# Optimization experiments

Measured on AMD Instinct MI355X. Metric: run time of the kernel, lower is better.

## Reference

```python
import jax, jax.numpy as jnp
import numpy as np

EPS = 1e-05


def _nearest_upsample(x, H, W):
    # torch F.interpolate default mode='nearest': src_idx = floor(dst_idx * in/out)
    h, w = x.shape[-2], x.shape[-1]
    rows = (jnp.arange(H) * h) // H
    cols = (jnp.arange(W) * w) // W
    return x[..., rows[:, None], cols[None, :]]


def _dilate(mask, k):
    # Grayscale dilation with a flat (all-ones) k x k structuring element ==
    # k x k max filter (kornia dilation w/ ones kernel). Geodesic border: pad -inf
    p = (k - 1) // 2
    return jax.lax.reduce_window(
        mask, -jnp.inf, jax.lax.max,
        window_dimensions=(1, 1, k, k),
        window_strides=(1, 1, 1, 1),
        padding=[(0, 0), (0, 0), (p, k - 1 - p), (p, k - 1 - p)],
    )


def setup_inputs() -> dict:
    key = jax.random.key(0)
    k1, k2 = jax.random.split(key)
    small = jax.random.normal(k1, (2, 4, 1, 270, 480), dtype=jnp.float32)
    large = jax.random.uniform(k2, (2, 4, 1, 1080, 1920), dtype=jnp.float32)
    return {"small": small, "large": large, "dilate_width": 7, "sigmoid": 1}


def reference(small, large, dilate_width, sigmoid):
    B, T = small.shape[0], small.shape[1]
    s = small.reshape((B * T,) + small.shape[2:])   # [BT, C, h, w]
    l = large.reshape((B * T,) + large.shape[2:])   # [BT, C, H, W]
    H, W = l.shape[-2], l.shape[-1]
    up = _nearest_upsample(s, H, W)
    t = jax.nn.sigmoid(up) if sigmoid else up
    trans = ((t > EPS) & (t < 1.0 - EPS)).astype(l.dtype)
    if dilate_width >= 1:
        trans = _dilate(trans, dilate_width)
    out = trans * l + (1.0 - trans) * up
    return out.reshape(large.shape)
```

## Files before the change

### kernel.cpp

```cpp
#include <hip/hip_runtime.h>
#include <cmath>

#define HS 270
#define WS 480
#define HL 1080
#define WL 1920
#define W4 (WL / 4)

typedef float f4 __attribute__((ext_vector_type(4)));

__global__ __launch_bounds__(256) void PRM_77824807403842_kernel(
    const float* __restrict__ sml,
    const float* __restrict__ lrg,
    const int* __restrict__ sigp,
    float* __restrict__ out)
{
    const int n2 = blockIdx.x * 256 + threadIdx.x;
    const int bt = blockIdx.z;
    const int i = n2 / W4;
    const int p = n2 - i * W4;
    const int q = i >> 2;
    const int s = i & 3;

    const size_t lofs = ((size_t)bt * HL + i) * WL + 4 * (size_t)p;
    const f4 lv = *reinterpret_cast<const f4*>(lrg + lofs);

    const float* sb = sml + (size_t)bt * (HS * WS);
    const int rm = q > 0 ? q - 1 : 0;
    const int rp = q < HS - 1 ? q + 1 : q;
    const int cm = p > 0 ? p - 1 : 0;
    const int cp = p < WS - 1 ? p + 1 : p;
    const unsigned inc_t = (unsigned)((s < 3) & (q > 0));
    const unsigned inc_b = (unsigned)((s > 0) & (q < HS - 1));
    const unsigned vl = p > 0, vr = p < WS - 1;

    const float* r0 = sb + (size_t)rm * WS;
    const float* r1 = sb + (size_t)q * WS;
    const float* r2 = sb + (size_t)rp * WS;
    const float a0 = r0[cm], a1 = r0[p], a2 = r0[cp];
    const float b0 = r1[cm], b1 = r1[p], b2 = r1[cp];
    const float c0 = r2[cm], c1 = r2[p], c2 = r2[cp];

    const int sig = *sigp;
    auto msk = [&](float x) -> unsigned {
        return sig ? (unsigned)((x > -11.5129154f) & (x < 11.5129054f))
                   : (unsigned)((x > 1e-5f) & (x < 0.99999f));
    };

    const unsigned Ml = ((inc_t & msk(a0)) | msk(b0) | (inc_b & msk(c0))) & vl;
    const unsigned Mm =  (inc_t & msk(a1)) | msk(b1) | (inc_b & msk(c1));
    const unsigned Mr = ((inc_t & msk(a2)) | msk(b2) | (inc_b & msk(c2))) & vr;

    const float up = b1;
    const unsigned L = Ml | Mm, A = L | Mr, R = Mm | Mr;
    f4 o;
    o.x = L ? lv.x : up;
    o.y = A ? lv.y : up;
    o.z = A ? lv.z : up;
    o.w = R ? lv.w : up;
    *reinterpret_cast<f4*>(out + lofs) = o;
}

extern "C" void kernel_launch(void* const* d_in, const int* in_sizes, int n_in,
                              void* d_out, int out_size, void* d_ws, size_t ws_size,
                              hipStream_t stream) {
    const float* sml = (const float*)d_in[0];
    const float* lrg = (const float*)d_in[1];
    const int* sigp = (const int*)d_in[3];
    float* outp = (float*)d_out;

    const int BT = in_sizes[1] / (HL * WL);

    dim3 grid(HL * W4 / 256, 1, BT);
    dim3 block(256);
    hipLaunchKernelGGL(PRM_77824807403842_kernel, grid, block, 0, stream,
                       sml, lrg, sigp, outp);
}
```

Before: 28.56 us.

## Use grid-stride persistent loop with software-pipelined prefetch of next element

Replaces the one-thread-per-vector grid with a fixed grid of 2048 blocks that stride over all elements. Each thread loads the large vector and nine small-tensor neighbours for its next element before computing and storing the current one, so loads overlap with compute and stores. This cuts block launch overhead but holds two stages of live registers and adds per-iteration index division, which may lower occupancy on a bandwidth-bound kernel.

```diff
diff --git a/kernel.cpp b/kernel.cpp
--- a/kernel.cpp
+++ b/kernel.cpp
@@ -6,59 +6,89 @@
 #define HL 1080
 #define WL 1920
 #define W4 (WL / 4)
+#define GPF (HL * W4)
 
 typedef float f4 __attribute__((ext_vector_type(4)));
 
-__global__ __launch_bounds__(256) void PRM_77824807403842_kernel(
-    const float* __restrict__ sml,
-    const float* __restrict__ lrg,
-    const int* __restrict__ sigp,
-    float* __restrict__ out)
-{
-    const int n2 = blockIdx.x * 256 + threadIdx.x;
-    const int bt = blockIdx.z;
-    const int i = n2 / W4;
-    const int p = n2 - i * W4;
-    const int q = i >> 2;
-    const int s = i & 3;
+struct Stage {
+    f4 lv;
+    float a0, a1, a2, b0, b1, b2, c0, c1, c2;
+    size_t lofs;
+    int q, s, p;
+};
 
-    const size_t lofs = ((size_t)bt * HL + i) * WL + 4 * (size_t)p;
-    const f4 lv = *reinterpret_cast<const f4*>(lrg + lofs);
+__device__ __forceinline__ void load_stage(const float* __restrict__ sml,
+                                           const float* __restrict__ lrg,
+                                           int g, Stage& S) {
+    const int bt = g / GPF;
+    const int r  = g - bt * GPF;
+    const int i  = r / W4;
+    const int p  = r - i * W4;
+    const int q  = i >> 2;
+    S.q = q; S.s = i & 3; S.p = p;
+
+    S.lofs = ((size_t)bt * HL + i) * WL + 4 * (size_t)p;
+    S.lv = *reinterpret_cast<const f4*>(lrg + S.lofs);
 
     const float* sb = sml + (size_t)bt * (HS * WS);
     const int rm = q > 0 ? q - 1 : 0;
     const int rp = q < HS - 1 ? q + 1 : q;
     const int cm = p > 0 ? p - 1 : 0;
     const int cp = p < WS - 1 ? p + 1 : p;
-    const unsigned inc_t = (unsigned)((s < 3) & (q > 0));
-    const unsigned inc_b = (unsigned)((s > 0) & (q < HS - 1));
-    const unsigned vl = p > 0, vr = p < WS - 1;
-
     const float* r0 = sb + (size_t)rm * WS;
     const float* r1 = sb + (size_t)q * WS;
     const float* r2 = sb + (size_t)rp * WS;
-    const float a0 = r0[cm], a1 = r0[p], a2 = r0[cp];
-    const float b0 = r1[cm], b1 = r1[p], b2 = r1[cp];
-    const float c0 = r2[cm], c1 = r2[p], c2 = r2[cp];
+    S.a0 = r0[cm]; S.a1 = r0[p]; S.a2 = r0[cp];
+    S.b0 = r1[cm]; S.b1 = r1[p]; S.b2 = r1[cp];
+    S.c0 = r2[cm]; S.c1 = r2[p]; S.c2 = r2[cp];
+}
 
-    const int sig = *sigp;
+__device__ __forceinline__ void compute_store(const Stage& S, int sig,
+                                              float* __restrict__ out) {
     auto msk = [&](float x) -> unsigned {
         return sig ? (unsigned)((x > -11.5129154f) & (x < 11.5129054f))
                    : (unsigned)((x > 1e-5f) & (x < 0.99999f));
     };
+    const unsigned inc_t = (unsigned)((S.s < 3) & (S.q > 0));
+    const unsigned inc_b = (unsigned)((S.s > 0) & (S.q < HS - 1));
+    const unsigned vl = S.p > 0, vr = S.p < WS - 1;
 
-    const unsigned Ml = ((inc_t & msk(a0)) | msk(b0) | (inc_b & msk(c0))) & vl;
-    const unsigned Mm =  (inc_t & msk(a1)) | msk(b1) | (inc_b & msk(c1));
-    const unsigned Mr = ((inc_t & msk(a2)) | msk(b2) | (inc_b & msk(c2))) & vr;
+    const unsigned Ml = ((inc_t & msk(S.a0)) | msk(S.b0) | (inc_b & msk(S.c0))) & vl;
+    const unsigned Mm =  (inc_t & msk(S.a1)) | msk(S.b1) | (inc_b & msk(S.c1));
+    const unsigned Mr = ((inc_t & msk(S.a2)) | msk(S.b2) | (inc_b & msk(S.c2))) & vr;
 
-    const float up = b1;
+    const float up = S.b1;
     const unsigned L = Ml | Mm, A = L | Mr, R = Mm | Mr;
     f4 o;
-    o.x = L ? lv.x : up;
-    o.y = A ? lv.y : up;
-    o.z = A ? lv.z : up;
-    o.w = R ? lv.w : up;
-    *reinterpret_cast<f4*>(out + lofs) = o;
+    o.x = L ? S.lv.x : up;
+    o.y = A ? S.lv.y : up;
+    o.z = A ? S.lv.z : up;
+    o.w = R ? S.lv.w : up;
+    *reinterpret_cast<f4*>(out + S.lofs) = o;
+}
+
+__global__ __launch_bounds__(256) void PRM_77824807403842_kernel(
+    const float* __restrict__ sml,
+    const float* __restrict__ lrg,
+    const int* __restrict__ sigp,
+    float* __restrict__ out,
+    int G, int NB)
+{
+    const int sig = *sigp;
+    int g = blockIdx.x * 256 + threadIdx.x;
+    if (g >= G) return;
+
+    Stage cur;
+    load_stage(sml, lrg, g, cur);
+    int gn = g + NB;
+    while (gn < G) {
+        Stage nxt;
+        load_stage(sml, lrg, gn, nxt);
+        compute_store(cur, sig, out);
+        cur = nxt;
+        gn += NB;
+    }
+    compute_store(cur, sig, out);
 }
 
 extern "C" void kernel_launch(void* const* d_in, const int* in_sizes, int n_in,
@@ -70,9 +100,12 @@
     float* outp = (float*)d_out;
 
     const int BT = in_sizes[1] / (HL * WL);
+    const int G = BT * GPF;
+    const int NBLK = 2048;
+    const int NB = NBLK * 256;
 
-    dim3 grid(HL * W4 / 256, 1, BT);
+    dim3 grid(NBLK, 1, 1);
     dim3 block(256);
     hipLaunchKernelGGL(PRM_77824807403842_kernel, grid, block, 0, stream,
-                       sml, lrg, sigp, outp);
+                       sml, lrg, sigp, outp, G, NB);
 }
```

Result: slower. 31.09 us (+8.9%).
